# Optimization experiments

Hardware: AMD Instinct MI355X
Metric: run time of the kernel (lower is better)

Reference implementation:

```python
import jax, jax.numpy as jnp
import numpy as np

N_NODES = 100000
N_EDGES = 800000
NODE_DIM = 128
HIDDEN = 256
OUT_DIM = 512
N_LAYERS = 4
N_GRAPHS = 64


def _linear_init(key, out_f, in_f):
    kw, kb = jax.random.split(key)
    bound = 1.0 / np.sqrt(in_f)
    w = jax.random.uniform(kw, (out_f, in_f), jnp.float32, -bound, bound)
    b = jax.random.uniform(kb, (out_f,), jnp.float32, -bound, bound)
    return w, b


def setup_inputs() -> dict:
    key = jax.random.key(0)
    ks = jax.random.split(key, 16)
    x = jax.random.normal(ks[0], (N_NODES, NODE_DIM), jnp.float32)
    edge_index = jax.random.randint(ks[1], (2, N_EDGES), 0, N_NODES, jnp.int64)
    batch = jnp.sort(jax.random.randint(ks[2], (N_NODES,), 0, N_GRAPHS, jnp.int64))
    node_w, node_b = _linear_init(ks[3], HIDDEN, NODE_DIM)
    gw1, gb1, gw2, gb2 = [], [], [], []
    for i in range(N_LAYERS):
        w1, b1 = _linear_init(ks[4 + 2 * i], HIDDEN, HIDDEN)
        w2, b2 = _linear_init(ks[5 + 2 * i], HIDDEN, HIDDEN)
        gw1.append(w1); gb1.append(b1); gw2.append(w2); gb2.append(b2)
    gin_w1 = jnp.stack(gw1); gin_b1 = jnp.stack(gb1)
    gin_w2 = jnp.stack(gw2); gin_b2 = jnp.stack(gb2)
    eps = jnp.zeros((N_LAYERS,), jnp.float32)  # train_eps init 0
    out_w1, out_b1 = _linear_init(ks[12], HIDDEN, HIDDEN)
    out_w2, out_b2 = _linear_init(ks[13], OUT_DIM, HIDDEN)
    return {
        "x": x, "edge_index": edge_index, "batch": batch,
        "node_w": node_w, "node_b": node_b,
        "gin_w1": gin_w1, "gin_b1": gin_b1,
        "gin_w2": gin_w2, "gin_b2": gin_b2, "eps": eps,
        "out_w1": out_w1, "out_b1": out_b1,
        "out_w2": out_w2, "out_b2": out_b2,
    }


def reference(x, edge_index, batch, node_w, node_b, gin_w1, gin_b1, gin_w2,
              gin_b2, eps, out_w1, out_b1, out_w2, out_b2):
    src, dst = edge_index[0], edge_index[1]
    # node projection + relu
    h = jax.nn.relu(x @ node_w.T + node_b)  # [N, H]
    for i in range(N_LAYERS):
        # GINConv: mlp((1+eps)*x + sum_{j in N(i)} x_j); x_j = h[src], agg at dst
        agg = jax.ops.segment_sum(h[src], dst, num_segments=N_NODES)
        z = (1.0 + eps[i]) * h + agg
        z = jax.nn.relu(z @ gin_w1[i].T + gin_b1[i])
        z = z @ gin_w2[i].T + gin_b2[i]
        h = jax.nn.relu(z)  # outer relu in forward
    # global_mean_pool over batch assignment
    counts = jax.ops.segment_sum(jnp.ones((N_NODES,), h.dtype), batch,
                                 num_segments=N_GRAPHS)
    sums = jax.ops.segment_sum(h, batch, num_segments=N_GRAPHS)
    h_graph = sums / jnp.maximum(counts, 1.0)[:, None]  # [B, H]
    out = jax.nn.relu(h_graph @ out_w1.T + out_b1) @ out_w2.T + out_b2
    return out  # [B, OUT_DIM]
```

## Files before the change

### kernel.cpp

```cpp
#include <hip/hip_runtime.h>
#include <stdint.h>

#define N_NODES   100000
#define N_EDGES   800000
#define NODE_DIM  128
#define HIDDEN    256
#define OUT_DIM   512
#define N_LAYERS  4
#define N_GRAPHS  64
#define POOL_CHUNKS 8
#define SCAN_BLK  1024
#define SCAN_NB   ((N_NODES + SCAN_BLK - 1) / SCAN_BLK)

typedef _Float16 f16;
typedef __attribute__((ext_vector_type(8))) _Float16 f16x8;
typedef __attribute__((ext_vector_type(4))) _Float16 f16x4;
typedef __attribute__((ext_vector_type(4))) float    f32x4;

__global__ void k_f2h(const float* __restrict__ in, f16* __restrict__ out, int n4) {
    int i = blockIdx.x * 256 + threadIdx.x;
    if (i < n4) {
        f32x4 v = *(const f32x4*)(in + (size_t)i * 4);
        f16x4 o;
        o[0] = (f16)v[0]; o[1] = (f16)v[1]; o[2] = (f16)v[2]; o[3] = (f16)v[3];
        *(f16x4*)(out + (size_t)i * 4) = o;
    }
}

__global__ void k_hist(const int* __restrict__ ei, int* __restrict__ deg) {
    int e = blockIdx.x * 256 + threadIdx.x;
    if (e < N_EDGES) atomicAdd(&deg[ei[N_EDGES + e]], 1);
}

__global__ __launch_bounds__(1024) void k_scan1(const int* __restrict__ deg,
                                                int* __restrict__ rowptr,
                                                int* __restrict__ bsums) {
    __shared__ int tmp[SCAN_BLK];
    int tid = threadIdx.x;
    int i = blockIdx.x * SCAN_BLK + tid;
    int v = (i < N_NODES) ? deg[i] : 0;
    tmp[tid] = v;
    __syncthreads();
    for (int off = 1; off < SCAN_BLK; off <<= 1) {
        int t = (tid >= off) ? tmp[tid - off] : 0;
        __syncthreads();
        tmp[tid] += t;
        __syncthreads();
    }
    if (i < N_NODES) rowptr[i] = tmp[tid] - v;
    if (tid == SCAN_BLK - 1) bsums[blockIdx.x] = tmp[tid];
}

__global__ __launch_bounds__(128) void k_scan2(const int* __restrict__ bsums,
                                               int* __restrict__ boffs,
                                               int* __restrict__ rowptr) {
    __shared__ int tmp[128];
    int tid = threadIdx.x;
    int v = (tid < SCAN_NB) ? bsums[tid] : 0;
    tmp[tid] = v;
    __syncthreads();
    for (int off = 1; off < 128; off <<= 1) {
        int t = (tid >= off) ? tmp[tid - off] : 0;
        __syncthreads();
        tmp[tid] += t;
        __syncthreads();
    }
    if (tid < SCAN_NB) boffs[tid] = tmp[tid] - v;
    if (tid == 127) rowptr[N_NODES] = tmp[127];
}

__global__ __launch_bounds__(1024) void k_scan3(int* __restrict__ rowptr,
                                                const int* __restrict__ boffs,
                                                int* __restrict__ cursor) {
    int i = blockIdx.x * SCAN_BLK + threadIdx.x;
    if (i < N_NODES) {
        int r = rowptr[i] + boffs[blockIdx.x];
        rowptr[i] = r;
        cursor[i] = r;
    }
}

__global__ void k_scatter(const int* __restrict__ ei, int* __restrict__ cursor,
                          int* __restrict__ col) {
    int e = blockIdx.x * 256 + threadIdx.x;
    if (e < N_EDGES) {
        int d = ei[N_EDGES + e];
        int p = atomicAdd(&cursor[d], 1);
        col[p] = ei[e];
    }
}

__global__ __launch_bounds__(256) void k_agg(const f16* __restrict__ h,
                                             const int* __restrict__ rowptr,
                                             const int* __restrict__ col,
                                             const float* __restrict__ eps, int layer,
                                             f16* __restrict__ z) {
    int node = blockIdx.x * 4 + (threadIdx.x >> 6);
    if (node >= N_NODES) return;
    int lane = threadIdx.x & 63;
    int c0 = lane * 4;
    float e1 = 1.0f + eps[layer];
    f16x4 hv = *(const f16x4*)(h + (size_t)node * HIDDEN + c0);
    float a0 = e1 * (float)hv[0], a1 = e1 * (float)hv[1];
    float a2 = e1 * (float)hv[2], a3 = e1 * (float)hv[3];
    int jb = rowptr[node], je = rowptr[node + 1];
    int j = jb;
    for (; j + 4 <= je; j += 4) {
        int s0 = col[j], s1 = col[j + 1], s2 = col[j + 2], s3 = col[j + 3];
        f16x4 v0 = *(const f16x4*)(h + (size_t)s0 * HIDDEN + c0);
        f16x4 v1 = *(const f16x4*)(h + (size_t)s1 * HIDDEN + c0);
        f16x4 v2 = *(const f16x4*)(h + (size_t)s2 * HIDDEN + c0);
        f16x4 v3 = *(const f16x4*)(h + (size_t)s3 * HIDDEN + c0);
        a0 += (float)v0[0] + (float)v1[0] + (float)v2[0] + (float)v3[0];
        a1 += (float)v0[1] + (float)v1[1] + (float)v2[1] + (float)v3[1];
        a2 += (float)v0[2] + (float)v1[2] + (float)v2[2] + (float)v3[2];
        a3 += (float)v0[3] + (float)v1[3] + (float)v2[3] + (float)v3[3];
    }
    for (; j < je; ++j) {
        int s = col[j];
        f16x4 v = *(const f16x4*)(h + (size_t)s * HIDDEN + c0);
        a0 += (float)v[0]; a1 += (float)v[1]; a2 += (float)v[2]; a3 += (float)v[3];
    }
    f16x4 o;
    o[0] = (f16)a0; o[1] = (f16)a1; o[2] = (f16)a2; o[3] = (f16)a3;
    *(f16x4*)(z + (size_t)node * HIDDEN + c0) = o;
}

template<int K>
__global__ __launch_bounds__(512) void k_gemm(const f16* __restrict__ A,
                                              const f16* __restrict__ B,
                                              const float* __restrict__ bias,
                                              f16* __restrict__ C, int nsl16) {
    constexpr int NPANEL = K >> 6;
    constexpr int NKS    = K >> 5;
    __shared__ f16 Bs[NPANEL * 256 * 64];
    const int tid = threadIdx.x, wid = tid >> 6, lane = tid & 63;
    const int klo = lane >> 4;
    const int l15 = lane & 15;

#pragma unroll
    for (int p = 0; p < NPANEL; ++p) {
#pragma unroll
        for (int r = 0; r < 4; ++r) {
            int chunk = (r << 9) + tid;
            int brow = chunk >> 3, c8 = chunk & 7;
            int sc8  = c8 ^ (brow & 7);
            const f16* src = B + (size_t)brow * K + (p << 6) + sc8 * 8;
            f16* dst = Bs + (p << 14) + (size_t)((r << 9) + (wid << 6)) * 8;
            __builtin_amdgcn_global_load_lds((const __attribute__((address_space(1))) void*)src,
                                             (__attribute__((address_space(3))) void*)dst, 16, 0, 0);
        }
    }
    __syncthreads();

    auto loada = [&](f16x8 (&a)[NKS], int slab) {
        const f16* arow = A + (size_t)((slab << 4) + l15) * K + (klo << 3);
#pragma unroll
        for (int ks = 0; ks < NKS; ++ks)
            a[ks] = *(const f16x8*)(arow + (ks << 5));
    };
    auto compute = [&](const f16x8 (&a)[NKS], int slab) {
        f32x4 acc[16] = {};
#pragma unroll
        for (int ks = 0; ks < NKS; ++ks) {
            const int kk = ((ks & 1) << 2) | klo;
            const f16* pb = Bs + ((ks >> 1) << 14);
#pragma unroll
            for (int n = 0; n < 16; ++n) {
                int rb = (n << 4) + l15;
                f16x8 bf = *(const f16x8*)(pb + rb * 64 + ((kk ^ (rb & 7)) << 3));
                acc[n] = __builtin_amdgcn_mfma_f32_16x16x32_f16(a[ks], bf, acc[n], 0, 0, 0);
            }
        }
#pragma unroll
        for (int n = 0; n < 16; ++n) {
            int gc = (n << 4) + l15;
            float bv = bias[gc];
#pragma unroll
            for (int j = 0; j < 4; ++j) {
                int gr = (slab << 4) + (klo << 2) + j;
                float v = fmaxf(acc[n][j] + bv, 0.0f);
                C[(size_t)gr * HIDDEN + gc] = (f16)v;
            }
        }
    };

    const int STRIDE = gridDim.x * 8;
    int s = blockIdx.x * 8 + wid;
    if (s >= nsl16) return;
    f16x8 aA[NKS], aB[NKS];
    loada(aA, s);
    for (;;) {
        int s2 = s + STRIDE;
        if (s2 < nsl16) loada(aB, s2);
        compute(aA, s);
        if (s2 >= nsl16) break;
        int s3 = s2 + STRIDE;
        if (s3 < nsl16) loada(aA, s3);
        compute(aB, s2);
        if (s3 >= nsl16) break;
        s = s3;
    }
}

__global__ void k_bounds(const int* __restrict__ batch, int* __restrict__ starts) {
    int i = blockIdx.x * 256 + threadIdx.x;
    if (i >= N_NODES) return;
    int g  = batch[i];
    int gp = (i == 0) ? -1 : batch[i - 1];
    for (int q = gp + 1; q <= g; ++q) starts[q] = i;
    if (i == N_NODES - 1) {
        for (int q = g + 1; q <= N_GRAPHS; ++q) starts[q] = N_NODES;
    }
}

__global__ __launch_bounds__(256) void k_pool(const f16* __restrict__ h,
                                              const int* __restrict__ starts,
                                              float* __restrict__ part) {
    int g = blockIdx.x, ch = blockIdx.y, c = threadIdx.x;
    int s = starts[g], e = starts[g + 1];
    int len = e - s;
    int per = (len + POOL_CHUNKS - 1) / POOL_CHUNKS;
    int lo = s + ch * per;
    int hi = lo + per; if (hi > e) hi = e;
    float acc = 0.0f;
    for (int n = lo; n < hi; ++n) acc += (float)h[(size_t)n * HIDDEN + c];
    part[((size_t)g * POOL_CHUNKS + ch) * HIDDEN + c] = acc;
}

__global__ __launch_bounds__(256) void k_head(const float* __restrict__ part,
                                              const int* __restrict__ starts,
                                              const float* __restrict__ w1,
                                              const float* __restrict__ b1,
                                              const float* __restrict__ w2,
                                              const float* __restrict__ b2,
                                              float* __restrict__ out) {
    __shared__ float hg[HIDDEN];
    __shared__ float t[HIDDEN];
    int g = blockIdx.x, tid = threadIdx.x;
    int cnti = starts[g + 1] - starts[g];
    float cnt = (float)(cnti > 1 ? cnti : 1);
    float s = 0.0f;
#pragma unroll
    for (int ch = 0; ch < POOL_CHUNKS; ++ch)
        s += part[((size_t)g * POOL_CHUNKS + ch) * HIDDEN + tid];
    hg[tid] = s / cnt;
    __syncthreads();
    float a = b1[tid];
    for (int k = 0; k < HIDDEN; ++k) a += hg[k] * w1[(size_t)tid * HIDDEN + k];
    t[tid] = fmaxf(a, 0.0f);
    __syncthreads();
    for (int j = tid; j < OUT_DIM; j += 256) {
        float o = b2[j];
        for (int k = 0; k < HIDDEN; ++k) o += t[k] * w2[(size_t)j * HIDDEN + k];
        out[(size_t)g * OUT_DIM + j] = o;
    }
}

extern "C" void kernel_launch(void* const* d_in, const int* in_sizes, int n_in,
                              void* d_out, int out_size, void* d_ws, size_t ws_size,
                              hipStream_t stream) {
    const float* x      = (const float*)d_in[0];
    const int*   ei     = (const int*)d_in[1];
    const int*   batch  = (const int*)d_in[2];
    const float* node_w = (const float*)d_in[3];
    const float* node_b = (const float*)d_in[4];
    const float* gw1    = (const float*)d_in[5];
    const float* gb1    = (const float*)d_in[6];
    const float* gw2    = (const float*)d_in[7];
    const float* gb2    = (const float*)d_in[8];
    const float* eps    = (const float*)d_in[9];
    const float* ow1    = (const float*)d_in[10];
    const float* ob1    = (const float*)d_in[11];
    const float* ow2    = (const float*)d_in[12];
    const float* ob2    = (const float*)d_in[13];
    float* out = (float*)d_out;

    char* p = (char*)d_ws;
    auto alloc = [&](size_t bytes) {
        char* r = p;
        p += (bytes + 255) & ~(size_t)255;
        return (void*)r;
    };
    f16* hb   = (f16*)alloc((size_t)N_NODES * HIDDEN * 2);
    f16* zb   = (f16*)alloc((size_t)N_NODES * HIDDEN * 2);
    f16* tb   = (f16*)alloc((size_t)N_NODES * HIDDEN * 2);
    f16* xb   = (f16*)alloc((size_t)N_NODES * NODE_DIM * 2);
    f16* nwb  = (f16*)alloc((size_t)HIDDEN * NODE_DIM * 2);
    f16* w1b  = (f16*)alloc((size_t)N_LAYERS * HIDDEN * HIDDEN * 2);
    f16* w2b  = (f16*)alloc((size_t)N_LAYERS * HIDDEN * HIDDEN * 2);
    int* deg    = (int*)alloc((size_t)N_NODES * 4);
    int* rowptr = (int*)alloc((size_t)(N_NODES + 1) * 4);
    int* cursor = (int*)alloc((size_t)N_NODES * 4);
    int* col    = (int*)alloc((size_t)N_EDGES * 4);
    float* part = (float*)alloc((size_t)N_GRAPHS * POOL_CHUNKS * HIDDEN * 4);
    int* starts = (int*)alloc((size_t)(N_GRAPHS + 1) * 4);
    int* bsums  = (int*)alloc((size_t)SCAN_NB * 4);
    int* boffs  = (int*)alloc((size_t)SCAN_NB * 4);
    (void)in_sizes; (void)n_in; (void)out_size; (void)ws_size;

    hipMemsetAsync(deg, 0, (size_t)N_NODES * 4, stream);

    k_f2h<<<(N_NODES * NODE_DIM / 4 + 255) / 256, 256, 0, stream>>>(x, xb, N_NODES * NODE_DIM / 4);
    k_f2h<<<(HIDDEN * NODE_DIM / 4 + 255) / 256, 256, 0, stream>>>(node_w, nwb, HIDDEN * NODE_DIM / 4);
    k_f2h<<<(N_LAYERS * HIDDEN * HIDDEN / 4 + 255) / 256, 256, 0, stream>>>(gw1, w1b, N_LAYERS * HIDDEN * HIDDEN / 4);
    k_f2h<<<(N_LAYERS * HIDDEN * HIDDEN / 4 + 255) / 256, 256, 0, stream>>>(gw2, w2b, N_LAYERS * HIDDEN * HIDDEN / 4);

    k_hist<<<(N_EDGES + 255) / 256, 256, 0, stream>>>(ei, deg);
    k_scan1<<<SCAN_NB, SCAN_BLK, 0, stream>>>(deg, rowptr, bsums);
    k_scan2<<<1, 128, 0, stream>>>(bsums, boffs, rowptr);
    k_scan3<<<SCAN_NB, SCAN_BLK, 0, stream>>>(rowptr, boffs, cursor);
    k_scatter<<<(N_EDGES + 255) / 256, 256, 0, stream>>>(ei, cursor, col);

    k_bounds<<<(N_NODES + 255) / 256, 256, 0, stream>>>(batch, starts);

    const int NSL16 = N_NODES / 16;
    k_gemm<NODE_DIM><<<256, 512, 0, stream>>>(xb, nwb, node_b, hb, NSL16);

    for (int l = 0; l < N_LAYERS; ++l) {
        k_agg<<<(N_NODES + 3) / 4, 256, 0, stream>>>(hb, rowptr, col, eps, l, zb);
        k_gemm<HIDDEN><<<256, 512, 0, stream>>>(zb, w1b + (size_t)l * HIDDEN * HIDDEN,
                                                gb1 + (size_t)l * HIDDEN, tb, NSL16);
        k_gemm<HIDDEN><<<256, 512, 0, stream>>>(tb, w2b + (size_t)l * HIDDEN * HIDDEN,
                                                gb2 + (size_t)l * HIDDEN, hb, NSL16);
    }

    dim3 pgrid(N_GRAPHS, POOL_CHUNKS);
    k_pool<<<pgrid, 256, 0, stream>>>(hb, starts, part);
    k_head<<<N_GRAPHS, 256, 0, stream>>>(part, starts, ow1, ob1, ow2, ob2, out);
}
```

Baseline: 701.5 us.

## Fuse neighbor aggregation into first GIN MLP GEMM

Replaces the separate aggregation kernel and first GEMM with a single kernel. Each wave gathers neighbor rows for its 16-row slice directly into the MFMA A-fragment layout, converts to f16 and multiplies against the LDS-resident weights. This removes the write and re-read of the intermediate z buffer in every layer. In exchange, the gather now runs on a fixed 256-block grid with 16 rows per wave whose neighbor loops diverge by degree, which may reduce the latency hiding for the irregular loads.

```diff
diff --git a/kernel.cpp b/kernel.cpp
--- a/kernel.cpp
+++ b/kernel.cpp
@@ -90,40 +90,93 @@
     }
 }
 
-__global__ __launch_bounds__(256) void k_agg(const f16* __restrict__ h,
-                                             const int* __restrict__ rowptr,
-                                             const int* __restrict__ col,
-                                             const float* __restrict__ eps, int layer,
-                                             f16* __restrict__ z) {
-    int node = blockIdx.x * 4 + (threadIdx.x >> 6);
-    if (node >= N_NODES) return;
-    int lane = threadIdx.x & 63;
-    int c0 = lane * 4;
-    float e1 = 1.0f + eps[layer];
-    f16x4 hv = *(const f16x4*)(h + (size_t)node * HIDDEN + c0);
-    float a0 = e1 * (float)hv[0], a1 = e1 * (float)hv[1];
-    float a2 = e1 * (float)hv[2], a3 = e1 * (float)hv[3];
-    int jb = rowptr[node], je = rowptr[node + 1];
-    int j = jb;
-    for (; j + 4 <= je; j += 4) {
-        int s0 = col[j], s1 = col[j + 1], s2 = col[j + 2], s3 = col[j + 3];
-        f16x4 v0 = *(const f16x4*)(h + (size_t)s0 * HIDDEN + c0);
-        f16x4 v1 = *(const f16x4*)(h + (size_t)s1 * HIDDEN + c0);
-        f16x4 v2 = *(const f16x4*)(h + (size_t)s2 * HIDDEN + c0);
-        f16x4 v3 = *(const f16x4*)(h + (size_t)s3 * HIDDEN + c0);
-        a0 += (float)v0[0] + (float)v1[0] + (float)v2[0] + (float)v3[0];
-        a1 += (float)v0[1] + (float)v1[1] + (float)v2[1] + (float)v3[1];
-        a2 += (float)v0[2] + (float)v1[2] + (float)v2[2] + (float)v3[2];
-        a3 += (float)v0[3] + (float)v1[3] + (float)v2[3] + (float)v3[3];
-    }
-    for (; j < je; ++j) {
-        int s = col[j];
-        f16x4 v = *(const f16x4*)(h + (size_t)s * HIDDEN + c0);
-        a0 += (float)v[0]; a1 += (float)v[1]; a2 += (float)v[2]; a3 += (float)v[3];
-    }
-    f16x4 o;
-    o[0] = (f16)a0; o[1] = (f16)a1; o[2] = (f16)a2; o[3] = (f16)a3;
-    *(f16x4*)(z + (size_t)node * HIDDEN + c0) = o;
+__global__ __launch_bounds__(512) void k_aggemm(const f16* __restrict__ h,
+                                                const int* __restrict__ rowptr,
+                                                const int* __restrict__ col,
+                                                const float* __restrict__ eps, int layer,
+                                                const f16* __restrict__ W,
+                                                const float* __restrict__ bias,
+                                                f16* __restrict__ T, int nsl16) {
+    constexpr int K = HIDDEN;
+    constexpr int NPANEL = K >> 6;
+    constexpr int NKS    = K >> 5;
+    __shared__ f16 Bs[NPANEL * 256 * 64];
+    const int tid = threadIdx.x, wid = tid >> 6, lane = tid & 63;
+    const int klo = lane >> 4;
+    const int l15 = lane & 15;
+
+#pragma unroll
+    for (int p = 0; p < NPANEL; ++p) {
+#pragma unroll
+        for (int r = 0; r < 4; ++r) {
+            int chunk = (r << 9) + tid;
+            int brow = chunk >> 3, c8 = chunk & 7;
+            int sc8  = c8 ^ (brow & 7);
+            const f16* src = W + (size_t)brow * K + (p << 6) + sc8 * 8;
+            f16* dst = Bs + (p << 14) + (size_t)((r << 9) + (wid << 6)) * 8;
+            __builtin_amdgcn_global_load_lds((const __attribute__((address_space(1))) void*)src,
+                                             (__attribute__((address_space(3))) void*)dst, 16, 0, 0);
+        }
+    }
+    __syncthreads();
+    const float e1 = 1.0f + eps[layer];
+
+    for (int s = blockIdx.x * 8 + wid; s < nsl16; s += (gridDim.x << 3)) {
+        const int row = (s << 4) + l15;
+        float zacc[NKS][8];
+        {
+            const f16* hrow = h + (size_t)row * HIDDEN + (klo << 3);
+            f16x8 v[NKS];
+#pragma unroll
+            for (int ks = 0; ks < NKS; ++ks) v[ks] = *(const f16x8*)(hrow + (ks << 5));
+#pragma unroll
+            for (int ks = 0; ks < NKS; ++ks)
+#pragma unroll
+                for (int q = 0; q < 8; ++q) zacc[ks][q] = e1 * (float)v[ks][q];
+        }
+        int jb = rowptr[row], je = rowptr[row + 1];
+        for (int j = jb; j < je; ++j) {
+            const f16* prow = h + (size_t)col[j] * HIDDEN + (klo << 3);
+            f16x8 v[NKS];
+#pragma unroll
+            for (int ks = 0; ks < NKS; ++ks) v[ks] = *(const f16x8*)(prow + (ks << 5));
+#pragma unroll
+            for (int ks = 0; ks < NKS; ++ks)
+#pragma unroll
+                for (int q = 0; q < 8; ++q) zacc[ks][q] += (float)v[ks][q];
+        }
+        f16x8 a[NKS];
+#pragma unroll
+        for (int ks = 0; ks < NKS; ++ks) {
+            f16x8 t;
+#pragma unroll
+            for (int q = 0; q < 8; ++q) t[q] = (f16)zacc[ks][q];
+            a[ks] = t;
+        }
+        f32x4 acc[16] = {};
+#pragma unroll
+        for (int ks = 0; ks < NKS; ++ks) {
+            const int kk = ((ks & 1) << 2) | klo;
+            const f16* pb = Bs + ((ks >> 1) << 14);
+#pragma unroll
+            for (int n = 0; n < 16; ++n) {
+                int rb = (n << 4) + l15;
+                f16x8 bf = *(const f16x8*)(pb + rb * 64 + ((kk ^ (rb & 7)) << 3));
+                acc[n] = __builtin_amdgcn_mfma_f32_16x16x32_f16(a[ks], bf, acc[n], 0, 0, 0);
+            }
+        }
+#pragma unroll
+        for (int n = 0; n < 16; ++n) {
+            int gc = (n << 4) + l15;
+            float bv = bias[gc];
+#pragma unroll
+            for (int j = 0; j < 4; ++j) {
+                int gr = (s << 4) + (klo << 2) + j;
+                float v = fmaxf(acc[n][j] + bv, 0.0f);
+                T[(size_t)gr * HIDDEN + gc] = (f16)v;
+            }
+        }
+    }
 }
 
 template<int K>
@@ -283,7 +336,6 @@
         return (void*)r;
     };
     f16* hb   = (f16*)alloc((size_t)N_NODES * HIDDEN * 2);
-    f16* zb   = (f16*)alloc((size_t)N_NODES * HIDDEN * 2);
     f16* tb   = (f16*)alloc((size_t)N_NODES * HIDDEN * 2);
     f16* xb   = (f16*)alloc((size_t)N_NODES * NODE_DIM * 2);
     f16* nwb  = (f16*)alloc((size_t)HIDDEN * NODE_DIM * 2);
@@ -318,9 +370,9 @@
     k_gemm<NODE_DIM><<<256, 512, 0, stream>>>(xb, nwb, node_b, hb, NSL16);
 
     for (int l = 0; l < N_LAYERS; ++l) {
-        k_agg<<<(N_NODES + 3) / 4, 256, 0, stream>>>(hb, rowptr, col, eps, l, zb);
-        k_gemm<HIDDEN><<<256, 512, 0, stream>>>(zb, w1b + (size_t)l * HIDDEN * HIDDEN,
-                                                gb1 + (size_t)l * HIDDEN, tb, NSL16);
+        k_aggemm<<<256, 512, 0, stream>>>(hb, rowptr, col, eps, l,
+                                          w1b + (size_t)l * HIDDEN * HIDDEN,
+                                          gb1 + (size_t)l * HIDDEN, tb, NSL16);
         k_gemm<HIDDEN><<<256, 512, 0, stream>>>(tb, w2b + (size_t)l * HIDDEN * HIDDEN,
                                                 gb2 + (size_t)l * HIDDEN, hb, NSL16);
     }
```

Measured after the change: 1.572 ms. 124% more time.
